# Kernel optimization log

Hardware: AMD Instinct MI355X
Metric: run time of the kernel (lower is better)

Reference implementation:

```python
import jax, jax.numpy as jnp
import numpy as np

E, KD, VD = 1024, 1024, 1024
B, S = 4, 4096


def setup_inputs() -> dict:
    key = jax.random.key(0)
    ks = jax.random.split(key, 7)
    sE, sK = 1.0 / np.sqrt(E), 1.0 / np.sqrt(E)
    return {
        "x": jax.random.normal(ks[0], (B, S, E), dtype=jnp.float32),
        "Wq": jax.random.normal(ks[1], (E, KD), dtype=jnp.float32) * sE,
        "bq": jnp.zeros((KD,), dtype=jnp.float32),
        "Wk": jax.random.normal(ks[2], (E, KD), dtype=jnp.float32) * sE,
        "bk": jnp.zeros((KD,), dtype=jnp.float32),
        "Wv": jax.random.normal(ks[3], (E, VD), dtype=jnp.float32) * sE,
        "bv": jnp.zeros((VD,), dtype=jnp.float32),
    }


def reference(x, Wq, bq, Wk, bk, Wv, bv):
    # Separate Q/K/V projections (nn.Linear equivalents)
    Q = jnp.einsum("bse,ek->bsk", x, Wq) + bq  # [B,S,KD]
    K = jnp.einsum("bse,ek->bsk", x, Wk) + bk  # [B,S,KD]
    V = jnp.einsum("bse,ev->bsv", x, Wv) + bv  # [B,S,VD]
    scale = 1.0 / jnp.sqrt(jnp.float32(KD))
    scores = jnp.einsum("bqk,bsk->bqs", Q, K) * scale  # [B,S,S]
    attn = jax.nn.softmax(scores, axis=-1)
    out = jnp.einsum("bqs,bsv->bqv", attn, V)  # [B,S,VD]
    return out
```

## Files before the change

### kernel.cpp

```cpp
#include <hip/hip_runtime.h>
#include <cstdint>
#include <math.h>

typedef __attribute__((ext_vector_type(8))) short short8;
typedef __attribute__((ext_vector_type(4))) float f32x4;

#define AS1C const __attribute__((address_space(1))) void*
#define AS3  __attribute__((address_space(3))) void*

__device__ __forceinline__ unsigned short f2bf(float f) {
  union { float f; unsigned int u; } v; v.f = f;
  unsigned int r = v.u + 0x7FFFu + ((v.u >> 16) & 1u);
  return (unsigned short)(r >> 16);
}

__global__ void cast_x_kernel(const float* __restrict__ x, unsigned short* __restrict__ xb) {
  int i = blockIdx.x * blockDim.x + threadIdx.x;
  float4 v = ((const float4*)x)[i];
  ushort4 o;
  o.x = f2bf(v.x); o.y = f2bf(v.y); o.z = f2bf(v.z); o.w = f2bf(v.w);
  ((ushort4*)xb)[i] = o;
}

__global__ void zero_f4_kernel(float4* __restrict__ o) {
  size_t i = (size_t)blockIdx.x * blockDim.x + threadIdx.x;
  float4 z; z.x = 0.f; z.y = 0.f; z.z = 0.f; z.w = 0.f;
  o[i] = z;
}

__global__ void transpose_cast_kernel(const float* __restrict__ W0, const float* __restrict__ W1,
                                      const float* __restrict__ W2,
                                      unsigned short* __restrict__ T0, unsigned short* __restrict__ T1,
                                      unsigned short* __restrict__ T2) {
  __shared__ float tile[32][33];
  const float* W = (blockIdx.z == 0) ? W0 : (blockIdx.z == 1 ? W1 : W2);
  unsigned short* T = (blockIdx.z == 0) ? T0 : (blockIdx.z == 1 ? T1 : T2);
  int tx = threadIdx.x & 31, ty = threadIdx.x >> 5;
  int bx = blockIdx.x * 32, by = blockIdx.y * 32;
#pragma unroll
  for (int i = 0; i < 32; i += 8)
    tile[ty + i][tx] = W[(size_t)(by + ty + i) * 1024 + bx + tx];
  __syncthreads();
#pragma unroll
  for (int i = 0; i < 32; i += 8)
    T[(size_t)(bx + ty + i) * 1024 + by + tx] = f2bf(tile[tx][ty + i]);
}

template <int KDIM, int NT>
__device__ __forceinline__ void gemm_core8(const unsigned short* __restrict__ Abase,
                                           const unsigned short* __restrict__ Btbase,
                                           unsigned short* smem, f32x4 acc[8][4]) {
  const int t = threadIdx.x;
  const int lane = t & 63, wave = t >> 6;
  const int wm = wave >> 2, wn = wave & 3;
  const int quad = lane >> 4, l16 = lane & 15;

  const int row0 = t >> 3;
  const int gsw = (t & 7) ^ (row0 & 7);
  const unsigned short* gsrc =
      (gsw & 4) ? (Btbase + (size_t)row0 * KDIM + (size_t)(gsw - 4) * 8)
                : (Abase + (size_t)row0 * KDIM + (size_t)gsw * 8);

  auto stage2 = [&](int reg, int T, int pair) {
    unsigned short* buf = smem + reg * 16384;
    const unsigned short* s = gsrc + T * 32;
#pragma unroll
    for (int j2 = 0; j2 < 2; ++j2) {
      int j = pair * 2 + j2;
      __builtin_amdgcn_global_load_lds((AS1C)(s + (size_t)j * 64 * KDIM),
                                       (AS3)(buf + (t + j * 512) * 8), 16, 0, 0);
    }
  };
  auto rdA4 = [&](short8* a, int reg, int mb) {
    const unsigned short* buf = smem + reg * 16384;
#pragma unroll
    for (int i = 0; i < 4; ++i) {
      int row = wm * 128 + (mb + i) * 16 + l16;
      a[i] = *(const short8*)(buf + row * 64 + ((quad ^ (row & 7)) << 3));
    }
  };
  auto rdB4 = [&](short8* b, int reg) {
    const unsigned short* buf = smem + reg * 16384;
#pragma unroll
    for (int i = 0; i < 4; ++i) {
      int row = wn * 64 + i * 16 + l16;
      b[i] = *(const short8*)(buf + row * 64 + (((4 + quad) ^ (row & 7)) << 3));
    }
  };
  auto mf16 = [&](short8* a, short8* b, int mb) {
    __builtin_amdgcn_s_setprio(1);
#pragma unroll
    for (int mi = 0; mi < 4; ++mi)
#pragma unroll
      for (int ni = 0; ni < 4; ++ni)
        acc[mb + mi][ni] =
            __builtin_amdgcn_mfma_f32_16x16x32_bf16(a[mi], b[ni], acc[mb + mi][ni], 0, 0, 0);
    __builtin_amdgcn_s_setprio(0);
  };

#define BAR()   asm volatile("s_barrier" ::: "memory")
#define LGKM0() asm volatile("s_waitcnt lgkmcnt(0)" ::: "memory")
#define VM(N)   asm volatile("s_waitcnt vmcnt(" #N ")" ::: "memory")

  stage2(0, 0, 0); stage2(0, 0, 1);
  stage2(1, 1, 0); stage2(1, 1, 1);
  stage2(2, 2, 0); stage2(2, 2, 1);
  VM(8);
  BAR();

  short8 a0[4], a1[4], b0[4];
  for (int it = 0; it < NT / 4; ++it) {
    const int T = 4 * it;
    const bool lastI = (it == NT / 4 - 1);
    rdA4(a0, 0, 0); rdB4(b0, 0);
    stage2(3, T + 3, 0);
    BAR(); LGKM0();
    mf16(a0, b0, 0);
    BAR();
    rdA4(a1, 0, 4);
    stage2(3, T + 3, 1);
    VM(8);
    BAR(); LGKM0();
    mf16(a1, b0, 4);
    BAR();
    rdA4(a0, 1, 0); rdB4(b0, 1);
    if (!lastI) stage2(0, T + 4, 0);
    BAR(); LGKM0();
    mf16(a0, b0, 0);
    BAR();
    rdA4(a1, 1, 4);
    if (!lastI) { stage2(0, T + 4, 1); VM(8); }
    else        { VM(4); }
    BAR(); LGKM0();
    mf16(a1, b0, 4);
    BAR();
    rdA4(a0, 2, 0); rdB4(b0, 2);
    if (!lastI) stage2(1, T + 5, 0);
    BAR(); LGKM0();
    mf16(a0, b0, 0);
    BAR();
    rdA4(a1, 2, 4);
    if (!lastI) { stage2(1, T + 5, 1); VM(8); }
    else        { VM(0); }
    BAR(); LGKM0();
    mf16(a1, b0, 4);
    BAR();
    rdA4(a0, 3, 0); rdB4(b0, 3);
    if (!lastI) stage2(2, T + 6, 0);
    BAR(); LGKM0();
    mf16(a0, b0, 0);
    BAR();
    rdA4(a1, 3, 4);
    if (!lastI) { stage2(2, T + 6, 1); VM(8); }
    BAR(); LGKM0();
    mf16(a1, b0, 4);
    BAR();
  }
#undef BAR
#undef LGKM0
#undef VM
}

struct ProjArgs {
  const unsigned short* bt[3];
  const float* bias[3];
  unsigned short* c[3];
};
struct SPairArgs {
  const unsigned short* q[2];
  const unsigned short* k[2];
  unsigned short* pc[2][4];
  float* rs[2];
};
struct PVPairArgs {
  const unsigned short* pc[2][4];
  const unsigned short* vt[2];
  const float* rs[2];
  float* out[2];
};

__global__ __launch_bounds__(512, 2) void gemm256_proj(
    const unsigned short* __restrict__ A, ProjArgs pa) {
  extern __shared__ unsigned short smem[];
  const int t = threadIdx.x;
  const int lane = t & 63, wave = t >> 6;
  const int wm = wave >> 2, wn = wave & 3;
  const int quad = lane >> 4, l16 = lane & 15;
  const int z = blockIdx.z;

  const int gx = gridDim.x;
  const int nwg = gx * gridDim.y;
  int bid = blockIdx.y * gx + blockIdx.x;
  bid = (bid & 7) * (nwg >> 3) + (bid >> 3);
  const int bx = bid % gx, by = bid / gx;
  const int m0 = bx * 256, n0 = by * 256;

  f32x4 acc[8][4];
  const f32x4 fz = {0.f, 0.f, 0.f, 0.f};
#pragma unroll
  for (int mi = 0; mi < 8; ++mi)
#pragma unroll
    for (int ni = 0; ni < 4; ++ni) acc[mi][ni] = fz;

  gemm_core8<1024, 32>(A + (size_t)m0 * 1024, pa.bt[z] + (size_t)n0 * 1024, smem, acc);

  const float* bias = pa.bias[z];
  unsigned short* C = pa.c[z];
  const float scale = (z == 0) ? 0.03125f : 1.0f;
  if (z < 2) {
#pragma unroll
    for (int mi = 0; mi < 8; ++mi) {
      int row = m0 + wm * 128 + mi * 16 + quad * 4;
#pragma unroll
      for (int ni = 0; ni < 4; ++ni) {
        int col = n0 + wn * 64 + ni * 16 + l16;
        float bv = bias[col];
#pragma unroll
        for (int r = 0; r < 4; ++r)
          C[(size_t)(row + r) * 1024 + col] = f2bf((acc[mi][ni][r] + bv) * scale);
      }
    }
  } else {
#pragma unroll
    for (int mi = 0; mi < 8; ++mi) {
      int row = m0 + wm * 128 + mi * 16 + quad * 4;
      int bb = row >> 12, ss = row & 4095;
#pragma unroll
      for (int ni = 0; ni < 4; ++ni) {
        int col = n0 + wn * 64 + ni * 16 + l16;
        float bv = bias[col];
        ushort4 pk;
        pk.x = f2bf(acc[mi][ni][0] + bv);
        pk.y = f2bf(acc[mi][ni][1] + bv);
        pk.z = f2bf(acc[mi][ni][2] + bv);
        pk.w = f2bf(acc[mi][ni][3] + bv);
        *(ushort4*)&C[((size_t)bb * 1024 + col) * 4096 + ss] = pk;
      }
    }
  }
}

__global__ __launch_bounds__(512, 2) void gemm256_s(SPairArgs sa) {
  extern __shared__ unsigned short smem[];
  const int t = threadIdx.x;
  const int lane = t & 63, wave = t >> 6;
  const int wm = wave >> 2, wn = wave & 3;
  const int quad = lane >> 4, l16 = lane & 15;
  const int z = blockIdx.z;

  const int gx = gridDim.x;
  const int nwg = gx * gridDim.y;
  int bid = blockIdx.y * gx + blockIdx.x;
  bid = (bid & 7) * (nwg >> 3) + (bid >> 3);
  const int bx = bid % gx, by = bid / gx;
  const int m0 = bx * 256, n0 = by * 256;

  f32x4 acc[8][4];
  const f32x4 fz = {0.f, 0.f, 0.f, 0.f};
#pragma unroll
  for (int mi = 0; mi < 8; ++mi)
#pragma unroll
    for (int ni = 0; ni < 4; ++ni) acc[mi][ni] = fz;

  gemm_core8<1024, 32>(sa.q[z] + (size_t)m0 * 1024, sa.k[z] + (size_t)n0 * 1024, smem, acc);

  unsigned short* base = sa.pc[z][m0 >> 10];
  float* rs = sa.rs[z];
#pragma unroll
  for (int mi = 0; mi < 8; ++mi) {
    int row = m0 + wm * 128 + mi * 16 + quad * 4;
    int rowl = row & 1023;
    float pr[4] = {0.f, 0.f, 0.f, 0.f};
#pragma unroll
    for (int ni = 0; ni < 4; ++ni) {
      int col = n0 + wn * 64 + ni * 16 + l16;
#pragma unroll
      for (int r = 0; r < 4; ++r) {
        float p = __expf(acc[mi][ni][r]);
        base[(size_t)(rowl + r) * 4096 + col] = f2bf(p);
        pr[r] += p;
      }
    }
#pragma unroll
    for (int r = 0; r < 4; ++r) {
      float v = pr[r];
      v += __shfl_xor(v, 1);
      v += __shfl_xor(v, 2);
      v += __shfl_xor(v, 4);
      v += __shfl_xor(v, 8);
      if (l16 == 0) atomicAdd(&rs[row + r], v);
    }
  }
}

__global__ __launch_bounds__(512, 2) void gemm256_pv(PVPairArgs va) {
  extern __shared__ unsigned short smem[];
  const int t = threadIdx.x;
  const int lane = t & 63, wave = t >> 6;
  const int wm = wave >> 2, wn = wave & 3;
  const int quad = lane >> 4, l16 = lane & 15;
  const int z = blockIdx.z;

  const int gx = gridDim.x, gy = gridDim.y;
  const int nwg = gx * gy;
  int lid = blockIdx.y * gx + blockIdx.x;
  int s = (lid & 7) * (nwg >> 3) + (lid >> 3);
  const int bx = s / gy, by = s % gy;
  const int m0 = bx * 256, n0 = by * 256;

  f32x4 acc[8][4];
  const f32x4 fz = {0.f, 0.f, 0.f, 0.f};
#pragma unroll
  for (int mi = 0; mi < 8; ++mi)
#pragma unroll
    for (int ni = 0; ni < 4; ++ni) acc[mi][ni] = fz;

  const unsigned short* Abase = va.pc[z][m0 >> 10] + (size_t)(m0 & 1023) * 4096;
  gemm_core8<4096, 128>(Abase, va.vt[z] + (size_t)n0 * 4096, smem, acc);

  const float* rs = va.rs[z];
  float* outp = va.out[z];
#pragma unroll
  for (int mi = 0; mi < 8; ++mi) {
    int row = m0 + wm * 128 + mi * 16 + quad * 4;
    float inv[4];
#pragma unroll
    for (int r = 0; r < 4; ++r) inv[r] = 1.0f / rs[row + r];
#pragma unroll
    for (int ni = 0; ni < 4; ++ni) {
      int col = n0 + wn * 64 + ni * 16 + l16;
#pragma unroll
      for (int r = 0; r < 4; ++r)
        outp[(size_t)(row + r) * 1024 + col] = acc[mi][ni][r] * inv[r];
    }
  }
}

extern "C" void kernel_launch(void* const* d_in, const int* in_sizes, int n_in,
                              void* d_out, int out_size, void* d_ws, size_t ws_size,
                              hipStream_t stream) {
  const float* x  = (const float*)d_in[0];
  const float* Wq = (const float*)d_in[1];
  const float* bq = (const float*)d_in[2];
  const float* Wk = (const float*)d_in[3];
  const float* bk = (const float*)d_in[4];
  const float* Wv = (const float*)d_in[5];
  const float* bv = (const float*)d_in[6];
  float* out = (float*)d_out;

  const size_t MR = (size_t)16384 * 1024;
  const size_t SB = (size_t)4096 * 1024;
  unsigned short* xb  = (unsigned short*)d_ws;
  unsigned short* Qb  = xb + MR;
  unsigned short* Kb  = Qb + MR;
  unsigned short* Vtb = Kb + MR;
  unsigned short* WqT = Vtb + MR;
  unsigned short* WkT = WqT + (size_t)1024 * 1024;
  unsigned short* WvT = WkT + (size_t)1024 * 1024;
  float* rs = (float*)WqT;
  unsigned short* outU = (unsigned short*)(out + (size_t)2 * 4096 * 1024);

  hipFuncSetAttribute((const void*)gemm256_proj,
                      hipFuncAttributeMaxDynamicSharedMemorySize, 131072);
  hipFuncSetAttribute((const void*)gemm256_s,
                      hipFuncAttributeMaxDynamicSharedMemorySize, 131072);
  hipFuncSetAttribute((const void*)gemm256_pv,
                      hipFuncAttributeMaxDynamicSharedMemorySize, 131072);

  cast_x_kernel<<<16384, 256, 0, stream>>>(x, xb);
  transpose_cast_kernel<<<dim3(32, 32, 3), 256, 0, stream>>>(Wq, Wk, Wv, WqT, WkT, WvT);

  ProjArgs pa;
  pa.bt[0] = WqT;  pa.bt[1] = WkT;  pa.bt[2] = WvT;
  pa.bias[0] = bq; pa.bias[1] = bk; pa.bias[2] = bv;
  pa.c[0] = Qb;    pa.c[1] = Kb;    pa.c[2] = Vtb;
  gemm256_proj<<<dim3(64, 4, 3), 512, 131072, stream>>>(xb, pa);

  zero_f4_kernel<<<16, 256, 0, stream>>>((float4*)rs);

  SPairArgs sA;
  sA.q[0] = Qb;      sA.k[0] = Kb;      sA.rs[0] = rs;
  sA.q[1] = Qb + SB; sA.k[1] = Kb + SB; sA.rs[1] = rs + 4096;
  for (int c = 0; c < 4; ++c) { sA.pc[0][c] = xb + (size_t)c * SB; sA.pc[1][c] = outU + (size_t)c * SB; }
  gemm256_s<<<dim3(16, 16, 2), 512, 131072, stream>>>(sA);

  PVPairArgs vA;
  for (int c = 0; c < 4; ++c) { vA.pc[0][c] = sA.pc[0][c]; vA.pc[1][c] = sA.pc[1][c]; }
  vA.vt[0] = Vtb;      vA.rs[0] = rs;        vA.out[0] = out;
  vA.vt[1] = Vtb + SB; vA.rs[1] = rs + 4096; vA.out[1] = out + (size_t)4096 * 1024;
  gemm256_pv<<<dim3(16, 4, 2), 512, 131072, stream>>>(vA);

  SPairArgs sB;
  sB.q[0] = Qb + 2 * SB; sB.k[0] = Kb + 2 * SB; sB.rs[0] = rs + 2 * 4096;
  sB.q[1] = Qb + 3 * SB; sB.k[1] = Kb + 3 * SB; sB.rs[1] = rs + 3 * 4096;
  for (int c = 0; c < 4; ++c) sB.pc[0][c] = xb + (size_t)c * SB;
  sB.pc[1][0] = Qb; sB.pc[1][1] = Qb + SB; sB.pc[1][2] = Kb; sB.pc[1][3] = Kb + SB;
  gemm256_s<<<dim3(16, 16, 2), 512, 131072, stream>>>(sB);

  PVPairArgs vB;
  for (int c = 0; c < 4; ++c) { vB.pc[0][c] = sB.pc[0][c]; vB.pc[1][c] = sB.pc[1][c]; }
  vB.vt[0] = Vtb + 2 * SB; vB.rs[0] = rs + 2 * 4096; vB.out[0] = out + (size_t)2 * 4096 * 1024;
  vB.vt[1] = Vtb + 3 * SB; vB.rs[1] = rs + 3 * 4096; vB.out[1] = out + (size_t)3 * 4096 * 1024;
  gemm256_pv<<<dim3(16, 4, 2), 512, 131072, stream>>>(vB);
}
```

Before: 578.7 us.

## Batch all four PV GEMMs into one launch when workspace allows

When the workspace is large enough, the change allocates two extra probability buffers so that all four batches' score/exp matrices can live in memory at once. It then runs both score kernels back to back and issues a single PV launch with z=4, rather than alternating two S and PV launches of z=2. The aim is fewer launches and a larger, better-filled PV grid with fewer tail effects. The cost is extra workspace, and the path depends on the harness providing enough of it; otherwise it falls back to the old schedule.

```diff
diff --git a/kernel.cpp b/kernel.cpp
--- a/kernel.cpp
+++ b/kernel.cpp
@@ -172,11 +172,11 @@
   unsigned short* pc[2][4];
   float* rs[2];
 };
-struct PVPairArgs {
-  const unsigned short* pc[2][4];
-  const unsigned short* vt[2];
-  const float* rs[2];
-  float* out[2];
+struct PVArgs {
+  const unsigned short* pc[4][4];
+  const unsigned short* vt[4];
+  const float* rs[4];
+  float* out[4];
 };
 
 __global__ __launch_bounds__(512, 2) void gemm256_proj(
@@ -293,7 +293,7 @@
   }
 }
 
-__global__ __launch_bounds__(512, 2) void gemm256_pv(PVPairArgs va) {
+__global__ __launch_bounds__(512, 2) void gemm256_pv(PVArgs va) {
   extern __shared__ unsigned short smem[];
   const int t = threadIdx.x;
   const int lane = t & 63, wave = t >> 6;
@@ -357,8 +357,13 @@
   unsigned short* WqT = Vtb + MR;
   unsigned short* WkT = WqT + (size_t)1024 * 1024;
   unsigned short* WvT = WkT + (size_t)1024 * 1024;
+  unsigned short* E1  = WvT + (size_t)1024 * 1024;
+  unsigned short* E2  = E1 + MR;
   float* rs = (float*)WqT;
   unsigned short* outU = (unsigned short*)(out + (size_t)2 * 4096 * 1024);
+
+  const size_t needA = ((size_t)(E2 + MR) - (size_t)d_ws);
+  const bool fullPV = (ws_size >= needA);
 
   hipFuncSetAttribute((const void*)gemm256_proj,
                       hipFuncAttributeMaxDynamicSharedMemorySize, 131072);
@@ -378,28 +383,57 @@
 
   zero_f4_kernel<<<16, 256, 0, stream>>>((float4*)rs);
 
-  SPairArgs sA;
-  sA.q[0] = Qb;      sA.k[0] = Kb;      sA.rs[0] = rs;
-  sA.q[1] = Qb + SB; sA.k[1] = Kb + SB; sA.rs[1] = rs + 4096;
-  for (int c = 0; c < 4; ++c) { sA.pc[0][c] = xb + (size_t)c * SB; sA.pc[1][c] = outU + (size_t)c * SB; }
-  gemm256_s<<<dim3(16, 16, 2), 512, 131072, stream>>>(sA);
-
-  PVPairArgs vA;
-  for (int c = 0; c < 4; ++c) { vA.pc[0][c] = sA.pc[0][c]; vA.pc[1][c] = sA.pc[1][c]; }
-  vA.vt[0] = Vtb;      vA.rs[0] = rs;        vA.out[0] = out;
-  vA.vt[1] = Vtb + SB; vA.rs[1] = rs + 4096; vA.out[1] = out + (size_t)4096 * 1024;
-  gemm256_pv<<<dim3(16, 4, 2), 512, 131072, stream>>>(vA);
-
-  SPairArgs sB;
-  sB.q[0] = Qb + 2 * SB; sB.k[0] = Kb + 2 * SB; sB.rs[0] = rs + 2 * 4096;
-  sB.q[1] = Qb + 3 * SB; sB.k[1] = Kb + 3 * SB; sB.rs[1] = rs + 3 * 4096;
-  for (int c = 0; c < 4; ++c) sB.pc[0][c] = xb + (size_t)c * SB;
-  sB.pc[1][0] = Qb; sB.pc[1][1] = Qb + SB; sB.pc[1][2] = Kb; sB.pc[1][3] = Kb + SB;
-  gemm256_s<<<dim3(16, 16, 2), 512, 131072, stream>>>(sB);
-
-  PVPairArgs vB;
-  for (int c = 0; c < 4; ++c) { vB.pc[0][c] = sB.pc[0][c]; vB.pc[1][c] = sB.pc[1][c]; }
-  vB.vt[0] = Vtb + 2 * SB; vB.rs[0] = rs + 2 * 4096; vB.out[0] = out + (size_t)2 * 4096 * 1024;
-  vB.vt[1] = Vtb + 3 * SB; vB.rs[1] = rs + 3 * 4096; vB.out[1] = out + (size_t)3 * 4096 * 1024;
-  gemm256_pv<<<dim3(16, 4, 2), 512, 131072, stream>>>(vB);
-}
+  if (fullPV) {
+    SPairArgs sA;
+    sA.q[0] = Qb;      sA.k[0] = Kb;      sA.rs[0] = rs;
+    sA.q[1] = Qb + SB; sA.k[1] = Kb + SB; sA.rs[1] = rs + 4096;
+    for (int c = 0; c < 4; ++c) { sA.pc[0][c] = xb + (size_t)c * SB; sA.pc[1][c] = E1 + (size_t)c * SB; }
+    gemm256_s<<<dim3(16, 16, 2), 512, 131072, stream>>>(sA);
+
+    SPairArgs sB;
+    sB.q[0] = Qb + 2 * SB; sB.k[0] = Kb + 2 * SB; sB.rs[0] = rs + 2 * 4096;
+    sB.q[1] = Qb + 3 * SB; sB.k[1] = Kb + 3 * SB; sB.rs[1] = rs + 3 * 4096;
+    sB.pc[0][0] = Qb; sB.pc[0][1] = Qb + SB; sB.pc[0][2] = Kb; sB.pc[0][3] = Kb + SB;
+    for (int c = 0; c < 4; ++c) sB.pc[1][c] = E2 + (size_t)c * SB;
+    gemm256_s<<<dim3(16, 16, 2), 512, 131072, stream>>>(sB);
+
+    PVArgs v;
+    for (int c = 0; c < 4; ++c) {
+      v.pc[0][c] = sA.pc[0][c];
+      v.pc[1][c] = sA.pc[1][c];
+      v.pc[2][c] = sB.pc[0][c];
+      v.pc[3][c] = sB.pc[1][c];
+    }
+    for (int b = 0; b < 4; ++b) {
+      v.vt[b] = Vtb + (size_t)b * SB;
+      v.rs[b] = rs + b * 4096;
+      v.out[b] = out + (size_t)b * 4096 * 1024;
+    }
+    gemm256_pv<<<dim3(16, 4, 4), 512, 131072, stream>>>(v);
+  } else {
+    SPairArgs sA;
+    sA.q[0] = Qb;      sA.k[0] = Kb;      sA.rs[0] = rs;
+    sA.q[1] = Qb + SB; sA.k[1] = Kb + SB; sA.rs[1] = rs + 4096;
+    for (int c = 0; c < 4; ++c) { sA.pc[0][c] = xb + (size_t)c * SB; sA.pc[1][c] = outU + (size_t)c * SB; }
+    gemm256_s<<<dim3(16, 16, 2), 512, 131072, stream>>>(sA);
+
+    PVArgs vA;
+    for (int c = 0; c < 4; ++c) { vA.pc[0][c] = sA.pc[0][c]; vA.pc[1][c] = sA.pc[1][c]; }
+    vA.vt[0] = Vtb;      vA.rs[0] = rs;        vA.out[0] = out;
+    vA.vt[1] = Vtb + SB; vA.rs[1] = rs + 4096; vA.out[1] = out + (size_t)4096 * 1024;
+    gemm256_pv<<<dim3(16, 4, 2), 512, 131072, stream>>>(vA);
+
+    SPairArgs sB;
+    sB.q[0] = Qb + 2 * SB; sB.k[0] = Kb + 2 * SB; sB.rs[0] = rs + 2 * 4096;
+    sB.q[1] = Qb + 3 * SB; sB.k[1] = Kb + 3 * SB; sB.rs[1] = rs + 3 * 4096;
+    for (int c = 0; c < 4; ++c) sB.pc[0][c] = xb + (size_t)c * SB;
+    sB.pc[1][0] = Qb; sB.pc[1][1] = Qb + SB; sB.pc[1][2] = Kb; sB.pc[1][3] = Kb + SB;
+    gemm256_s<<<dim3(16, 16, 2), 512, 131072, stream>>>(sB);
+
+    PVArgs vB;
+    for (int c = 0; c < 4; ++c) { vB.pc[0][c] = sB.pc[0][c]; vB.pc[1][c] = sB.pc[1][c]; }
+    vB.vt[0] = Vtb + 2 * SB; vB.rs[0] = rs + 2 * 4096; vB.out[0] = out + (size_t)2 * 4096 * 1024;
+    vB.vt[1] = Vtb + 3 * SB; vB.rs[1] = rs + 3 * 4096; vB.out[1] = out + (size_t)3 * 4096 * 1024;
+    gemm256_pv<<<dim3(16, 4, 2), 512, 131072, stream>>>(vB);
+  }
+}
```

Result: faster. 518.5 us (-10.4%).
